# Optimization experiments

Measured on AMD Instinct MI355X. Metric: run time of the kernel, lower is better.

The kernel has to match this reference:

```python
import jax, jax.numpy as jnp
import numpy as np

DIM = 1024
HEADS = 16
HEAD_DIM = DIM // HEADS
B, NQ, NK = 2, 2048, 2048


def setup_inputs() -> dict:
    key = jax.random.key(0)
    ks = jax.random.split(key, 8)
    s = 1.0 / np.sqrt(DIM)
    return {
        "query": jax.random.normal(ks[0], (B, NQ, DIM), jnp.float32),
        "key": jax.random.normal(ks[1], (B, NK, DIM), jnp.float32),
        "value": jax.random.normal(ks[2], (B, NK, DIM), jnp.float32),
        "qpos": jnp.zeros((B, NQ), jnp.int32),
        "kpos": jnp.zeros((B, NK), jnp.int32),
        "Wq": jax.random.normal(ks[3], (DIM, DIM), jnp.float32) * s,
        "Wk": jax.random.normal(ks[4], (DIM, DIM), jnp.float32) * s,
        "Wv": jax.random.normal(ks[5], (DIM, DIM), jnp.float32) * s,
        "Wo": jax.random.normal(ks[6], (DIM, DIM), jnp.float32) * s,
        "bo": jax.random.normal(ks[7], (DIM,), jnp.float32) * s,
    }


def reference(query, key, value, qpos, kpos, Wq, Wk, Wv, Wo, bo):
    # torch nn.Linear: y = x @ W.T (qkv_bias=False)
    Bq, Nq, C = query.shape
    Nk = key.shape[1]
    scale = HEAD_DIM ** -0.5
    # project and split heads: (B, H, N, Dh)
    q = (query @ Wq.T).reshape(Bq, Nq, HEADS, HEAD_DIM).transpose(0, 2, 1, 3)
    k = (key @ Wk.T).reshape(Bq, Nk, HEADS, HEAD_DIM).transpose(0, 2, 1, 3)
    v = (value @ Wv.T).reshape(Bq, Nk, HEADS, HEAD_DIM).transpose(0, 2, 1, 3)
    # rope is None, qk_norm False -> plain softmax attention
    attn = jnp.einsum("bhqd,bhkd->bhqk", q, k) * scale  # [B,H,Nq,Nk]
    attn = jax.nn.softmax(attn, axis=-1)
    x = jnp.einsum("bhqk,bhkd->bhqd", attn, v)
    x = x.transpose(0, 2, 1, 3).reshape(Bq, Nq, C)
    return x @ Wo.T + bo
```

## Files before the change

### kernel.cpp

```cpp
#include <hip/hip_runtime.h>
#include <hip/hip_bf16.h>
#include <stdint.h>

typedef __bf16 bf16_t;
typedef __bf16 bf16x4 __attribute__((ext_vector_type(4)));
typedef __bf16 bf16x8 __attribute__((ext_vector_type(8)));
typedef float  f32x4  __attribute__((ext_vector_type(4)));
typedef unsigned u32x2 __attribute__((ext_vector_type(2)));

#define MFMA16(a,b,c) __builtin_amdgcn_mfma_f32_16x16x32_bf16((a),(b),(c),0,0,0)

static constexpr int DIM = 1024, HEADS = 16, HD = 64, NB = 2, NQ = 2048, NKK = 2048;
static constexpr int MROWS = NB * NQ;
static constexpr float SCALE_Q = 0.18033688011112042f;

__global__ void cvt_all(const float* __restrict__ q, const float* __restrict__ k,
                        const float* __restrict__ v, const float* __restrict__ wq,
                        const float* __restrict__ wk, const float* __restrict__ wv,
                        const float* __restrict__ wo,
                        bf16_t* qb, bf16_t* kb, bf16_t* vb,
                        bf16_t* wqb, bf16_t* wkb, bf16_t* wvb, bf16_t* wob) {
  const int seg = blockIdx.y;
  const float* src; bf16_t* dst;
  size_t base;
  if (seg < 12) {
    int t = seg >> 2;
    src = t == 0 ? q : t == 1 ? k : v;
    dst = t == 0 ? qb : t == 1 ? kb : vb;
    base = (size_t)(seg & 3) * 262144;
  } else {
    int t = seg - 12;
    src = t == 0 ? wq : t == 1 ? wk : t == 2 ? wv : wo;
    dst = t == 0 ? wqb : t == 1 ? wkb : t == 2 ? wvb : wob;
    base = 0;
  }
  size_t i = base + blockIdx.x * 256 + threadIdx.x;
  float4 val = reinterpret_cast<const float4*>(src)[i];
  bf16x4 o;
  o[0] = (bf16_t)val.x; o[1] = (bf16_t)val.y; o[2] = (bf16_t)val.z; o[3] = (bf16_t)val.w;
  *reinterpret_cast<bf16x4*>(dst + i * 4) = o;
}

template<int ROWS, int TPB = 256>
__device__ __forceinline__ void stage_swz(const bf16_t* gbase, int gstride, bf16_t* lds, int tid) {
#pragma unroll
  for (int c = 0; c < ROWS * 8 / TPB; ++c) {
    int p = c * TPB + tid;
    int r = p >> 3, x = p & 7;
    const bf16_t* src = gbase + (size_t)r * gstride + ((x ^ (r & 7)) << 3);
    __builtin_amdgcn_global_load_lds(
        (const __attribute__((address_space(1))) void*)src,
        (__attribute__((address_space(3))) void*)(lds + (p << 3)),
        16, 0, 0);
  }
}

__device__ __forceinline__ bf16x8 lds_read8_swz(const bf16_t* lds, int row, int chunk) {
  int sc = chunk ^ (row & 7);
  return *reinterpret_cast<const bf16x8*>(lds + row * 64 + (sc << 3));
}

__device__ __forceinline__ unsigned cvtpk_bf16(float lo, float hi) {
  unsigned r;
  asm("v_cvt_pk_bf16_f32 %0, %1, %2" : "=v"(r) : "v"(lo), "v"(hi));
  return r;
}

__global__ __launch_bounds__(256) void gemm_qkv(const bf16_t* __restrict__ qb,
                                                const bf16_t* __restrict__ kb,
                                                const bf16_t* __restrict__ vb,
                                                const bf16_t* __restrict__ Wq,
                                                const bf16_t* __restrict__ Wk,
                                                const bf16_t* __restrict__ Wv,
                                                bf16_t* __restrict__ Qp,
                                                bf16_t* __restrict__ Kp,
                                                bf16_t* __restrict__ Vt) {
  constexpr int K = DIM, N = DIM;
  __shared__ __align__(16) bf16_t As[128 * 64];
  __shared__ __align__(16) bf16_t Bs[128 * 64];
  const int tid = threadIdx.x;
  const int lane = tid & 63, wid = tid >> 6;
  const int l15 = lane & 15, lg = lane >> 4;
  const int wr = wid >> 1, wc = wid & 1;
  const int bn = blockIdx.x, bm = blockIdx.y;
  const int sel = bn >> 3, bnl = bn & 7;

  const bf16_t* A  = sel == 0 ? qb : sel == 1 ? kb : vb;
  const bf16_t* Bt = sel == 0 ? Wq : sel == 1 ? Wk : Wv;
  const bf16_t* Abase = A + (size_t)(bm * 128) * K;
  const bf16_t* Bbase = Bt + (size_t)(bnl * 128) * K;

  f32x4 acc[4][4];
#pragma unroll
  for (int m = 0; m < 4; ++m)
#pragma unroll
    for (int n = 0; n < 4; ++n) acc[m][n] = (f32x4){0.f, 0.f, 0.f, 0.f};

  for (int k0 = 0; k0 < K; k0 += 64) {
    __syncthreads();
    stage_swz<128>(Abase + k0, K, As, tid);
    stage_swz<128>(Bbase + k0, K, Bs, tid);
    __syncthreads();
#pragma unroll
    for (int kk = 0; kk < 2; ++kk) {
      bf16x8 af[4], bfr[4];
#pragma unroll
      for (int m = 0; m < 4; ++m) af[m] = lds_read8_swz(As, wr * 64 + m * 16 + l15, kk * 4 + lg);
#pragma unroll
      for (int n = 0; n < 4; ++n) bfr[n] = lds_read8_swz(Bs, wc * 64 + n * 16 + l15, kk * 4 + lg);
#pragma unroll
      for (int m = 0; m < 4; ++m)
#pragma unroll
        for (int n = 0; n < 4; ++n)
          acc[m][n] = MFMA16(af[m], bfr[n], acc[m][n]);
    }
  }

  if (sel == 2) {
#pragma unroll
    for (int m = 0; m < 4; ++m) {
      int row0 = bm * 128 + wr * 64 + m * 16 + lg * 4;
      int bb = row0 >> 11, kv = row0 & 2047;
#pragma unroll
      for (int n = 0; n < 4; ++n) {
        int col = bnl * 128 + wc * 64 + n * 16 + l15;
        int hh = col >> 6, dd = col & 63;
        bf16x4 pk;
#pragma unroll
        for (int j = 0; j < 4; ++j) pk[j] = (bf16_t)acc[m][n][j];
        *reinterpret_cast<bf16x4*>(Vt + (((size_t)((bb * 16 + hh) * 64 + dd)) << 11) + kv) = pk;
      }
    }
  } else {
    bf16_t* Cout = sel == 0 ? Qp : Kp;
    const float scale = sel == 0 ? SCALE_Q : 1.0f;
#pragma unroll
    for (int m = 0; m < 4; ++m)
#pragma unroll
      for (int n = 0; n < 4; ++n)
#pragma unroll
        for (int j = 0; j < 4; ++j) {
          int row = bm * 128 + wr * 64 + m * 16 + lg * 4 + j;
          int col = bnl * 128 + wc * 64 + n * 16 + l15;
          Cout[(size_t)row * N + col] = (bf16_t)(acc[m][n][j] * scale);
        }
  }
}

__global__ __launch_bounds__(256) void gemm_out(const bf16_t* __restrict__ A,
                                                const bf16_t* __restrict__ Bt,
                                                float* __restrict__ Cout,
                                                const float* __restrict__ bias) {
  constexpr int K = DIM, N = DIM;
  __shared__ __align__(16) bf16_t As[128 * 64];
  __shared__ __align__(16) bf16_t Bs[128 * 64];
  const int tid = threadIdx.x;
  const int lane = tid & 63, wid = tid >> 6;
  const int l15 = lane & 15, lg = lane >> 4;
  const int wr = wid >> 1, wc = wid & 1;
  const int bn = blockIdx.x, bm = blockIdx.y;

  const bf16_t* Abase = A + (size_t)(bm * 128) * K;
  const bf16_t* Bbase = Bt + (size_t)(bn * 128) * K;

  f32x4 acc[4][4];
#pragma unroll
  for (int m = 0; m < 4; ++m)
#pragma unroll
    for (int n = 0; n < 4; ++n) acc[m][n] = (f32x4){0.f, 0.f, 0.f, 0.f};

  for (int k0 = 0; k0 < K; k0 += 64) {
    __syncthreads();
    stage_swz<128>(Abase + k0, K, As, tid);
    stage_swz<128>(Bbase + k0, K, Bs, tid);
    __syncthreads();
#pragma unroll
    for (int kk = 0; kk < 2; ++kk) {
      bf16x8 af[4], bfr[4];
#pragma unroll
      for (int m = 0; m < 4; ++m) af[m] = lds_read8_swz(As, wr * 64 + m * 16 + l15, kk * 4 + lg);
#pragma unroll
      for (int n = 0; n < 4; ++n) bfr[n] = lds_read8_swz(Bs, wc * 64 + n * 16 + l15, kk * 4 + lg);
#pragma unroll
      for (int m = 0; m < 4; ++m)
#pragma unroll
        for (int n = 0; n < 4; ++n)
          acc[m][n] = MFMA16(af[m], bfr[n], acc[m][n]);
    }
  }

#pragma unroll
  for (int m = 0; m < 4; ++m)
#pragma unroll
    for (int n = 0; n < 4; ++n)
#pragma unroll
      for (int j = 0; j < 4; ++j) {
        int row = bm * 128 + wr * 64 + m * 16 + lg * 4 + j;
        int col = bn * 128 + wc * 64 + n * 16 + l15;
        Cout[(size_t)row * N + col] = acc[m][n][j] + bias[col];
      }
}

__global__ __launch_bounds__(512) void attn_fused(const bf16_t* __restrict__ Qp,
                                                  const bf16_t* __restrict__ Kp,
                                                  const bf16_t* __restrict__ Vt,
                                                  bf16_t* __restrict__ Xa) {
  __shared__ __align__(16) bf16_t Ks[4][64 * 64];
  __shared__ __align__(16) bf16_t Vs[4][64 * 64];
  __shared__ __align__(16) bf16_t Ps[8][16 * 64];
  const int tid = threadIdx.x;
  const int lane = tid & 63, wid = tid >> 6;
  const int l15 = lane & 15, lg = lane >> 4;
  const int rot = (l15 & 7) * 8;

  int id = blockIdx.x + 16 * (blockIdx.y + 16 * blockIdx.z);
  int swz = (id & 7) * 64 + (id >> 3);
  const int bx = swz & 15, h = (swz >> 4) & 15, b = swz >> 8;
  const int q0 = bx * 128;

  const bf16_t* qbase = Qp + ((size_t)(b * NQ + q0)) * DIM + h * HD;
  const bf16_t* kbase = Kp + ((size_t)b * NKK) * DIM + h * HD;
  const bf16_t* vbase = Vt + ((size_t)((b * HEADS + h) * HD)) * NKK;

  stage_swz<128, 512>(qbase, DIM, &Ks[0][0], tid);
  __syncthreads();
  bf16x8 qf[2];
  qf[0] = lds_read8_swz(&Ks[0][0], wid * 16 + l15, lg);
  qf[1] = lds_read8_swz(&Ks[0][0], wid * 16 + l15, 4 + lg);
  __syncthreads();

  float m_ = -1e30f, l_ = 0.f;
  f32x4 o[4];
#pragma unroll
  for (int n = 0; n < 4; ++n) o[n] = (f32x4){0.f, 0.f, 0.f, 0.f};

  constexpr int NT = NKK / 64;

  stage_swz<64, 512>(kbase, DIM, &Ks[0][0], tid);
  stage_swz<64, 512>(vbase, NKK, &Vs[0][0], tid);
  stage_swz<64, 512>(kbase + (size_t)64 * DIM, DIM, &Ks[1][0], tid);
  stage_swz<64, 512>(vbase + 64, NKK, &Vs[1][0], tid);

  for (int t = 0; t < NT; t += 2) {
    if (t + 2 < NT) {
      stage_swz<64, 512>(kbase + (size_t)(t + 2) * 64 * DIM, DIM, &Ks[(t + 2) & 3][0], tid);
      stage_swz<64, 512>(vbase + (t + 2) * 64, NKK, &Vs[(t + 2) & 3][0], tid);
      stage_swz<64, 512>(kbase + (size_t)(t + 3) * 64 * DIM, DIM, &Ks[(t + 3) & 3][0], tid);
      stage_swz<64, 512>(vbase + (t + 3) * 64, NKK, &Vs[(t + 3) & 3][0], tid);
      asm volatile("s_waitcnt vmcnt(4)" ::: "memory");
    } else {
      asm volatile("s_waitcnt vmcnt(0)" ::: "memory");
    }
    __builtin_amdgcn_s_barrier();
    __builtin_amdgcn_sched_barrier(0);

#pragma unroll
    for (int u = 0; u < 2; ++u) {
      const int j = t + u;
      const bf16_t* kl = &Ks[j & 3][0];
      const bf16_t* vl = &Vs[j & 3][0];

      f32x4 scur[4];
      __builtin_amdgcn_s_setprio(1);
#pragma unroll
      for (int tt = 0; tt < 4; ++tt) {
        bf16x8 kf0 = lds_read8_swz(kl, tt * 16 + l15, lg);
        bf16x8 kf1 = lds_read8_swz(kl, tt * 16 + l15, 4 + lg);
        f32x4 a = (f32x4){0.f, 0.f, 0.f, 0.f};
        a = MFMA16(kf0, qf[0], a);
        a = MFMA16(kf1, qf[1], a);
        scur[tt] = a;
      }
      __builtin_amdgcn_s_setprio(0);

      float rm = scur[0][0];
#pragma unroll
      for (int tt = 0; tt < 4; ++tt)
#pragma unroll
        for (int jj = 0; jj < 4; ++jj) rm = fmaxf(rm, scur[tt][jj]);
      rm = fmaxf(rm, __shfl_xor(rm, 16));
      rm = fmaxf(rm, __shfl_xor(rm, 32));
      if (!__all(rm <= m_ + 8.f)) {
        float mn = fmaxf(m_, rm);
        float al = exp2f(m_ - mn);
        m_ = mn;
        l_ *= al;
#pragma unroll
        for (int n = 0; n < 4; ++n)
#pragma unroll
          for (int jj = 0; jj < 4; ++jj) o[n][jj] *= al;
      }
      float rs = 0.f;
#pragma unroll
      for (int tt = 0; tt < 4; ++tt)
#pragma unroll
        for (int jj = 0; jj < 4; ++jj) {
          float p = exp2f(scur[tt][jj] - m_);
          scur[tt][jj] = p;
          rs += p;
        }
      rs += __shfl_xor(rs, 16);
      rs += __shfl_xor(rs, 32);
      l_ += rs;

      bf16_t* Pw = &Ps[wid][0];
#pragma unroll
      for (int tt = 0; tt < 4; ++tt) {
        unsigned w0 = cvtpk_bf16(scur[tt][0], scur[tt][1]);
        unsigned w1 = cvtpk_bf16(scur[tt][2], scur[tt][3]);
        int col = (16 * tt + 4 * lg + rot) & 63;
        u32x2 pk2 = {w0, w1};
        *reinterpret_cast<u32x2*>(reinterpret_cast<char*>(Pw) + l15 * 128 + col * 2) = pk2;
      }
      asm volatile("s_waitcnt lgkmcnt(0)" ::: "memory");
      bf16x8 pf[2];
#pragma unroll
      for (int kt = 0; kt < 2; ++kt) {
        int col = (32 * kt + 8 * lg + rot) & 63;
        pf[kt] = *reinterpret_cast<const bf16x8*>(reinterpret_cast<const char*>(Pw) + l15 * 128 + col * 2);
      }

      __builtin_amdgcn_s_setprio(1);
#pragma unroll
      for (int n = 0; n < 4; ++n) {
#pragma unroll
        for (int kt = 0; kt < 2; ++kt) {
          bf16x8 vf = lds_read8_swz(vl, n * 16 + l15, 4 * kt + lg);
          o[n] = MFMA16(vf, pf[kt], o[n]);
        }
      }
      __builtin_amdgcn_s_setprio(0);
    }

    __builtin_amdgcn_s_barrier();
    __builtin_amdgcn_sched_barrier(0);
  }

  float inv = 1.f / l_;
  int q = q0 + wid * 16 + l15;
  bf16_t* ob = Xa + ((size_t)(b * NQ + q)) * DIM + h * HD;
#pragma unroll
  for (int n = 0; n < 4; ++n) {
    bf16x4 pk;
#pragma unroll
    for (int j = 0; j < 4; ++j) pk[j] = (bf16_t)(o[n][j] * inv);
    *reinterpret_cast<bf16x4*>(ob + n * 16 + 4 * lg) = pk;
  }
}

extern "C" void kernel_launch(void* const* d_in, const int* in_sizes, int n_in,
                              void* d_out, int out_size, void* d_ws, size_t ws_size,
                              hipStream_t stream) {
  (void)in_sizes; (void)n_in; (void)out_size; (void)ws_size;
  const float* q  = (const float*)d_in[0];
  const float* k  = (const float*)d_in[1];
  const float* v  = (const float*)d_in[2];
  const float* Wq = (const float*)d_in[5];
  const float* Wk = (const float*)d_in[6];
  const float* Wv = (const float*)d_in[7];
  const float* Wo = (const float*)d_in[8];
  const float* bo = (const float*)d_in[9];
  float* out = (float*)d_out;

  bf16_t* ws = (bf16_t*)d_ws;
  const size_t SZ_IN = (size_t)MROWS * DIM;
  const size_t SZ_W  = (size_t)DIM * DIM;
  bf16_t* qb  = ws;
  bf16_t* kb  = qb  + SZ_IN;
  bf16_t* vb  = kb  + SZ_IN;
  bf16_t* wqb = vb  + SZ_IN;
  bf16_t* wkb = wqb + SZ_W;
  bf16_t* wvb = wkb + SZ_W;
  bf16_t* wob = wvb + SZ_W;
  bf16_t* Qp  = wob + SZ_W;
  bf16_t* Kp  = Qp  + SZ_IN;
  bf16_t* Vtp = Kp  + SZ_IN;
  bf16_t* Xa  = qb;

  cvt_all<<<dim3(1024, 16), 256, 0, stream>>>(q, k, v, Wq, Wk, Wv, Wo,
                                              qb, kb, vb, wqb, wkb, wvb, wob);

  gemm_qkv<<<dim3(24, MROWS / 128), 256, 0, stream>>>(qb, kb, vb, wqb, wkb, wvb,
                                                      Qp, Kp, Vtp);

  attn_fused<<<dim3(NQ / 128, HEADS, NB), 512, 0, stream>>>(Qp, Kp, Vtp, Xa);

  gemm_out<<<dim3(DIM / 128, MROWS / 128), 256, 0, stream>>>(Xa, wob, out, bo);
}
```

Before: 152.9 us.

## Fuse fp32-to-bf16 activation conversion into QKV GEMM staging and remap block order

```diff
diff --git a/kernel.cpp b/kernel.cpp
--- a/kernel.cpp
+++ b/kernel.cpp
@@ -14,27 +14,13 @@
 static constexpr int MROWS = NB * NQ;
 static constexpr float SCALE_Q = 0.18033688011112042f;
 
-__global__ void cvt_all(const float* __restrict__ q, const float* __restrict__ k,
-                        const float* __restrict__ v, const float* __restrict__ wq,
-                        const float* __restrict__ wk, const float* __restrict__ wv,
-                        const float* __restrict__ wo,
-                        bf16_t* qb, bf16_t* kb, bf16_t* vb,
-                        bf16_t* wqb, bf16_t* wkb, bf16_t* wvb, bf16_t* wob) {
-  const int seg = blockIdx.y;
-  const float* src; bf16_t* dst;
-  size_t base;
-  if (seg < 12) {
-    int t = seg >> 2;
-    src = t == 0 ? q : t == 1 ? k : v;
-    dst = t == 0 ? qb : t == 1 ? kb : vb;
-    base = (size_t)(seg & 3) * 262144;
-  } else {
-    int t = seg - 12;
-    src = t == 0 ? wq : t == 1 ? wk : t == 2 ? wv : wo;
-    dst = t == 0 ? wqb : t == 1 ? wkb : t == 2 ? wvb : wob;
-    base = 0;
-  }
-  size_t i = base + blockIdx.x * 256 + threadIdx.x;
+__global__ void cvt_w(const float* __restrict__ wq, const float* __restrict__ wk,
+                      const float* __restrict__ wv, const float* __restrict__ wo,
+                      bf16_t* wqb, bf16_t* wkb, bf16_t* wvb, bf16_t* wob) {
+  const int t = blockIdx.y;
+  const float* src = t == 0 ? wq : t == 1 ? wk : t == 2 ? wv : wo;
+  bf16_t* dst = t == 0 ? wqb : t == 1 ? wkb : t == 2 ? wvb : wob;
+  size_t i = (size_t)blockIdx.x * 256 + threadIdx.x;
   float4 val = reinterpret_cast<const float4*>(src)[i];
   bf16x4 o;
   o[0] = (bf16_t)val.x; o[1] = (bf16_t)val.y; o[2] = (bf16_t)val.z; o[3] = (bf16_t)val.w;
@@ -55,6 +41,21 @@
   }
 }
 
+__device__ __forceinline__ void stage_f32(const float* gbase, int gstride, bf16_t* lds, int tid) {
+#pragma unroll
+  for (int c = 0; c < 4; ++c) {
+    int p = c * 256 + tid;
+    int r = p >> 3, x = p & 7;
+    const float* src = gbase + (size_t)r * gstride + ((x ^ (r & 7)) << 3);
+    float4 a = *reinterpret_cast<const float4*>(src);
+    float4 b2 = *reinterpret_cast<const float4*>(src + 4);
+    bf16x8 o;
+    o[0] = (bf16_t)a.x;  o[1] = (bf16_t)a.y;  o[2] = (bf16_t)a.z;  o[3] = (bf16_t)a.w;
+    o[4] = (bf16_t)b2.x; o[5] = (bf16_t)b2.y; o[6] = (bf16_t)b2.z; o[7] = (bf16_t)b2.w;
+    *reinterpret_cast<bf16x8*>(lds + (p << 3)) = o;
+  }
+}
+
 __device__ __forceinline__ bf16x8 lds_read8_swz(const bf16_t* lds, int row, int chunk) {
   int sc = chunk ^ (row & 7);
   return *reinterpret_cast<const bf16x8*>(lds + row * 64 + (sc << 3));
@@ -66,9 +67,9 @@
   return r;
 }
 
-__global__ __launch_bounds__(256) void gemm_qkv(const bf16_t* __restrict__ qb,
-                                                const bf16_t* __restrict__ kb,
-                                                const bf16_t* __restrict__ vb,
+__global__ __launch_bounds__(256) void gemm_qkv(const float* __restrict__ qf32,
+                                                const float* __restrict__ kf32,
+                                                const float* __restrict__ vf32,
                                                 const bf16_t* __restrict__ Wq,
                                                 const bf16_t* __restrict__ Wk,
                                                 const bf16_t* __restrict__ Wv,
@@ -82,12 +83,16 @@
   const int lane = tid & 63, wid = tid >> 6;
   const int l15 = lane & 15, lg = lane >> 4;
   const int wr = wid >> 1, wc = wid & 1;
-  const int bn = blockIdx.x, bm = blockIdx.y;
-  const int sel = bn >> 3, bnl = bn & 7;
-
-  const bf16_t* A  = sel == 0 ? qb : sel == 1 ? kb : vb;
+
+  int d = blockIdx.x + 24 * blockIdx.y;
+  int j = d & 7, rest = d >> 3;
+  int m_ = rest & 7, gq = rest >> 3;
+  int g = 8 * gq + j;
+  const int bm = g / 3, sel = g % 3, bnl = m_;
+
+  const float*  Af = sel == 0 ? qf32 : sel == 1 ? kf32 : vf32;
   const bf16_t* Bt = sel == 0 ? Wq : sel == 1 ? Wk : Wv;
-  const bf16_t* Abase = A + (size_t)(bm * 128) * K;
+  const float*  Abase = Af + (size_t)(bm * 128) * K;
   const bf16_t* Bbase = Bt + (size_t)(bnl * 128) * K;
 
   f32x4 acc[4][4];
@@ -98,7 +103,7 @@
 
   for (int k0 = 0; k0 < K; k0 += 64) {
     __syncthreads();
-    stage_swz<128>(Abase + k0, K, As, tid);
+    stage_f32(Abase + k0, K, As, tid);
     stage_swz<128>(Bbase + k0, K, Bs, tid);
     __syncthreads();
 #pragma unroll
@@ -127,7 +132,7 @@
         int hh = col >> 6, dd = col & 63;
         bf16x4 pk;
 #pragma unroll
-        for (int j = 0; j < 4; ++j) pk[j] = (bf16_t)acc[m][n][j];
+        for (int jj = 0; jj < 4; ++jj) pk[jj] = (bf16_t)acc[m][n][jj];
         *reinterpret_cast<bf16x4*>(Vt + (((size_t)((bb * 16 + hh) * 64 + dd)) << 11) + kv) = pk;
       }
     }
@@ -139,10 +144,10 @@
 #pragma unroll
       for (int n = 0; n < 4; ++n)
 #pragma unroll
-        for (int j = 0; j < 4; ++j) {
-          int row = bm * 128 + wr * 64 + m * 16 + lg * 4 + j;
+        for (int jj = 0; jj < 4; ++jj) {
+          int row = bm * 128 + wr * 64 + m * 16 + lg * 4 + jj;
           int col = bnl * 128 + wc * 64 + n * 16 + l15;
-          Cout[(size_t)row * N + col] = (bf16_t)(acc[m][n][j] * scale);
+          Cout[(size_t)row * N + col] = (bf16_t)(acc[m][n][jj] * scale);
         }
   }
 }
@@ -377,10 +382,9 @@
   bf16_t* Vtp = Kp  + SZ_IN;
   bf16_t* Xa  = qb;
 
-  cvt_all<<<dim3(1024, 16), 256, 0, stream>>>(q, k, v, Wq, Wk, Wv, Wo,
-                                              qb, kb, vb, wqb, wkb, wvb, wob);
-
-  gemm_qkv<<<dim3(24, MROWS / 128), 256, 0, stream>>>(qb, kb, vb, wqb, wkb, wvb,
+  cvt_w<<<dim3(1024, 4), 256, 0, stream>>>(Wq, Wk, Wv, Wo, wqb, wkb, wvb, wob);
+
+  gemm_qkv<<<dim3(24, MROWS / 128), 256, 0, stream>>>(q, k, v, wqb, wkb, wvb,
                                                       Qp, Kp, Vtp);
 
   attn_fused<<<dim3(NQ / 128, HEADS, NB), 512, 0, stream>>>(Qp, Kp, Vtp, Xa);
```

After: 151.6 us. About the same (-0.9%).
